# Optimization experiments

Measured on AMD Instinct MI355X. Metric: run time of the kernel, lower is better.

## Reference

```python
import jax, jax.numpy as jnp
import numpy as np

N_TOKENS = 16384
DIM = 7168
N_EXPERTS = 256
N_GROUPS = 8
TOPK_GROUPS = 4
TOPK = 8
ROUTE_SCALE = 2.5


def setup_inputs() -> dict:
    key = jax.random.key(0)
    k1, k2 = jax.random.split(key)
    x = jax.random.normal(k1, (N_TOKENS, DIM), dtype=jnp.float32)
    # kaiming_uniform_(a=sqrt(5)) -> Uniform(-1/sqrt(fan_in), 1/sqrt(fan_in))
    bound = 1.0 / np.sqrt(DIM)
    weight = jax.random.uniform(k2, (N_EXPERTS, DIM), dtype=jnp.float32,
                                minval=-bound, maxval=bound)
    expert_bias = jnp.zeros((N_EXPERTS,), dtype=jnp.float32)
    return {"x": x, "weight": weight, "expert_bias": expert_bias}


def reference(x, weight, expert_bias):
    n = x.shape[0]
    # linear scoring + sigmoid (score_func == 'sigmoid')
    scores = jax.nn.sigmoid(x @ weight.T)            # [n, E]
    biased = scores + expert_bias                    # [n, E]
    # group-limited routing
    bg = biased.reshape(n, N_GROUPS, -1)             # [n, G, E/G]
    top2, _ = jax.lax.top_k(bg, 2)
    group_scores = top2.sum(axis=-1)                 # [n, G]
    _, top_group_idx = jax.lax.top_k(group_scores, TOPK_GROUPS)  # [n, TOPK_GROUPS]
    keep = jax.nn.one_hot(top_group_idx, N_GROUPS, dtype=jnp.float32).sum(axis=1) > 0  # [n, G]
    masked = jnp.where(keep[:, :, None], bg, -jnp.inf).reshape(n, -1)  # [n, E]
    # final top-k over allowed experts
    _, indices = jax.lax.top_k(masked, TOPK)         # [n, TOPK]
    weights = jnp.take_along_axis(scores, indices, axis=1)
    weights = weights / (weights.sum(axis=-1, keepdims=True) + 1e-20)
    weights = weights * ROUTE_SCALE
    return weights.astype(x.dtype), indices
```

## Files before the change

kernel.cpp:

```cpp
#include <hip/hip_runtime.h>
#include <math.h>

#define MTOK 16384
#define NEXP 256
#define KDIM 7168

#define CAPR 1024
#define KSPLIT 8
#define KCH (KDIM / KSPLIT)
#define TAU 2e-5f

typedef _Float16 f16;
typedef __attribute__((ext_vector_type(8))) f16 f16x8;
typedef __attribute__((ext_vector_type(4))) f16 f16x4;
typedef __attribute__((ext_vector_type(4))) float f32x4;

#define BM 64
#define BN 128
#define BK 64
#define LDH 72

__launch_bounds__(256, 2)
__global__ void gemm_fp16x2_k(const float* __restrict__ X,
                              const float* __restrict__ W,
                              float* __restrict__ S) {
    __shared__ f16 Ahi[BM][LDH];
    __shared__ f16 Alo[BM][LDH];
    __shared__ f16 Bhi[BN][LDH];
    __shared__ f16 Blo[BN][LDH];

    const int tid  = threadIdx.x;
    const int lane = tid & 63;
    const int wid  = tid >> 6;
    const int wr   = wid >> 1;
    const int wc   = wid & 1;
    const int m0 = blockIdx.x * BM;
    const int n0 = blockIdx.y * BN;

    const int arow = tid >> 2;
    const int ac   = tid & 3;
    const int brow = tid >> 1;
    const int bc   = tid & 1;

    const float* xg = X + (size_t)(m0 + arow) * KDIM;
    const float* wg = W + (size_t)(n0 + brow) * KDIM;

    f32x4 accA[2][4];
    f32x4 accB[2][4];
#pragma unroll
    for (int i = 0; i < 2; ++i)
#pragma unroll
        for (int j = 0; j < 4; ++j) { accA[i][j] = (f32x4)0.f; accB[i][j] = (f32x4)0.f; }

    const int mr = wr * 32;
    const int nc = wc * 64;
    const int fr = lane & 15;
    const int fq = lane >> 4;

    for (int k0 = 0; k0 < KDIM; k0 += BK) {
        float4 av[4], bv[8];
#pragma unroll
        for (int i = 0; i < 4; ++i)
            av[i] = *(const float4*)(xg + k0 + (ac + i * 4) * 4);
#pragma unroll
        for (int i = 0; i < 8; ++i)
            bv[i] = *(const float4*)(wg + k0 + (bc + i * 2) * 4);

        __syncthreads();

#pragma unroll
        for (int i = 0; i < 4; ++i) {
            const int ke = (ac + i * 4) * 4;
            f16x4 h, l;
            h.x = (f16)av[i].x; l.x = (f16)((av[i].x - (float)h.x) * 2048.f);
            h.y = (f16)av[i].y; l.y = (f16)((av[i].y - (float)h.y) * 2048.f);
            h.z = (f16)av[i].z; l.z = (f16)((av[i].z - (float)h.z) * 2048.f);
            h.w = (f16)av[i].w; l.w = (f16)((av[i].w - (float)h.w) * 2048.f);
            *(f16x4*)&Ahi[arow][ke] = h;
            *(f16x4*)&Alo[arow][ke] = l;
        }
#pragma unroll
        for (int i = 0; i < 8; ++i) {
            const int ke = (bc + i * 2) * 4;
            f16x4 h, l;
            h.x = (f16)bv[i].x; l.x = (f16)((bv[i].x - (float)h.x) * 2048.f);
            h.y = (f16)bv[i].y; l.y = (f16)((bv[i].y - (float)h.y) * 2048.f);
            h.z = (f16)bv[i].z; l.z = (f16)((bv[i].z - (float)h.z) * 2048.f);
            h.w = (f16)bv[i].w; l.w = (f16)((bv[i].w - (float)h.w) * 2048.f);
            *(f16x4*)&Bhi[brow][ke] = h;
            *(f16x4*)&Blo[brow][ke] = l;
        }

        __syncthreads();

#pragma unroll
        for (int ks = 0; ks < 2; ++ks) {
            const int ke = ks * 32 + fq * 8;
            f16x8 ah[2], al[2], bh[4], bl[4];
#pragma unroll
            for (int mi = 0; mi < 2; ++mi) {
                ah[mi] = *(const f16x8*)&Ahi[mr + mi * 16 + fr][ke];
                al[mi] = *(const f16x8*)&Alo[mr + mi * 16 + fr][ke];
            }
#pragma unroll
            for (int ni = 0; ni < 4; ++ni) {
                bh[ni] = *(const f16x8*)&Bhi[nc + ni * 16 + fr][ke];
                bl[ni] = *(const f16x8*)&Blo[nc + ni * 16 + fr][ke];
            }
#pragma unroll
            for (int mi = 0; mi < 2; ++mi)
#pragma unroll
                for (int ni = 0; ni < 4; ++ni) {
                    accA[mi][ni] = __builtin_amdgcn_mfma_f32_16x16x32_f16(ah[mi], bh[ni], accA[mi][ni], 0, 0, 0);
                    accB[mi][ni] = __builtin_amdgcn_mfma_f32_16x16x32_f16(ah[mi], bl[ni], accB[mi][ni], 0, 0, 0);
                    accB[mi][ni] = __builtin_amdgcn_mfma_f32_16x16x32_f16(al[mi], bh[ni], accB[mi][ni], 0, 0, 0);
                }
        }
    }

#pragma unroll
    for (int mi = 0; mi < 2; ++mi)
#pragma unroll
        for (int ni = 0; ni < 4; ++ni) {
            const int e = n0 + nc + ni * 16 + fr;
#pragma unroll
            for (int r = 0; r < 4; ++r) {
                const int m = m0 + mr + mi * 16 + fq * 4 + r;
                float logit = accA[mi][ni][r] + accB[mi][ni][r] * (1.f / 2048.f);
                S[(size_t)m * NEXP + e] = 1.f / (1.f + expf(-logit));
            }
        }
}

__launch_bounds__(256)
__global__ void route_flag_k(const float* __restrict__ S,
                             const float* __restrict__ bias,
                             float* __restrict__ out,
                             int* __restrict__ list,
                             int* __restrict__ count) {
    __shared__ float sraw[4][256];
    const int wv   = threadIdx.x >> 6;
    const int lane = threadIdx.x & 63;
    const int token = blockIdx.x * 4 + wv;
    const float NINF = -__builtin_inff();
    const float PINF =  __builtin_inff();

    const float* row = S + (size_t)token * NEXP;
    float4 v = *(const float4*)(row + lane * 4);
    *(float4*)&sraw[wv][lane * 4] = v;

    const int e0 = lane * 4;
    float4 bi4 = *(const float4*)(bias + e0);
    float b0 = v.x + bi4.x;
    float b1 = v.y + bi4.y;
    float b2 = v.z + bi4.z;
    float b3 = v.w + bi4.w;

    bool flag = false;

    float m1 = b0, m2 = NINF;
    if (b1 > m1) { m2 = m1; m1 = b1; } else if (b1 > m2) m2 = b1;
    if (b2 > m1) { m2 = m1; m1 = b2; } else if (b2 > m2) m2 = b2;
    if (b3 > m1) { m2 = m1; m1 = b3; } else if (b3 > m2) m2 = b3;
#pragma unroll
    for (int w = 1; w <= 4; w <<= 1) {
        float o1 = __shfl_xor(m1, w);
        float o2 = __shfl_xor(m2, w);
        float nm1 = fmaxf(m1, o1);
        float nm2 = fmaxf(fminf(m1, o1), fmaxf(m2, o2));
        m1 = nm1; m2 = nm2;
    }
    const float gs = m1 + m2;
    const int g = lane >> 3;

    int rank = 0;
#pragma unroll
    for (int j = 0; j < 8; ++j) {
        float gj = __shfl(gs, j * 8);
        rank += (gj > gs) || (gj == gs && j < g);
    }
    const bool sel = rank < 4;

    {
        float a = sel ? gs : PINF;
        float b = sel ? NINF : gs;
#pragma unroll
        for (int w = 1; w < 64; w <<= 1) {
            a = fminf(a, __shfl_xor(a, w));
            b = fmaxf(b, __shfl_xor(b, w));
        }
        flag |= (a - b) < 2.f * TAU;
    }

    if (!sel) { b0 = NINF; b1 = NINF; b2 = NINF; b3 = NINF; }

    int myidx = 0;
    float prev = 0.f;
#pragma unroll
    for (int it = 0; it < 9; ++it) {
        float bv = b0; int bi = e0;
        if (b1 > bv) { bv = b1; bi = e0 + 1; }
        if (b2 > bv) { bv = b2; bi = e0 + 2; }
        if (b3 > bv) { bv = b3; bi = e0 + 3; }
#pragma unroll
        for (int w = 1; w < 64; w <<= 1) {
            float ov = __shfl_xor(bv, w);
            int   oi = __shfl_xor(bi, w);
            if (ov > bv || (ov == bv && oi < bi)) { bv = ov; bi = oi; }
        }
        if (it > 0) flag |= (prev - bv) < TAU;
        prev = bv;
        if (it < 8) {
            if (lane == it) myidx = bi;
            if ((bi >> 2) == lane) {
                switch (bi & 3) {
                    case 0: b0 = NINF; break;
                    case 1: b1 = NINF; break;
                    case 2: b2 = NINF; break;
                    case 3: b3 = NINF; break;
                }
            }
        }
    }

    const bool anyflag = __any((int)flag);

    __syncthreads();

    float wval = (lane < 8) ? sraw[wv][myidx] : 0.f;
    float s = wval;
    s += __shfl_xor(s, 1);
    s += __shfl_xor(s, 2);
    s += __shfl_xor(s, 4);
    if (lane < 8) {
        float wout = wval / (s + 1e-20f) * 2.5f;
        out[(size_t)token * 8 + lane] = wout;
        out[(size_t)MTOK * 8 + (size_t)token * 8 + lane] = (float)myidx;
    }

    if (anyflag && lane == 0) {
        int f = atomicAdd(count, 1);
        if (f < CAPR) list[f] = token;
    }
}

__launch_bounds__(256)
__global__ void rescore_k(const float* __restrict__ X,
                          const float* __restrict__ W,
                          const int* __restrict__ list,
                          const int* __restrict__ count,
                          double* __restrict__ Ldp) {
    const int cnt = min(*count, CAPR);
    const int m0 = blockIdx.x * 64;
    if (m0 >= cnt) return;
    const int n0 = blockIdx.y * 64;
    const int ks = blockIdx.z;
    const int kbase = ks * KCH;

    __shared__ float As[16][66];
    __shared__ float Bs[16][66];
    const int tid = threadIdx.x;
    const int row = tid >> 2;
    const int c   = tid & 3;
    const int tm  = tid >> 4;
    const int tn  = tid & 15;

    const int gi = list[min(m0 + row, cnt - 1)];
    const float* xg = X + (size_t)gi * KDIM + c * 4;
    const float* wg = W + (size_t)(n0 + row) * KDIM + c * 4;

    double acc[4][4];
#pragma unroll
    for (int i = 0; i < 4; ++i)
#pragma unroll
        for (int j = 0; j < 4; ++j) acc[i][j] = 0.0;

    for (int k0 = kbase; k0 < kbase + KCH; k0 += 16) {
        float4 a = *(const float4*)(xg + k0);
        float4 b = *(const float4*)(wg + k0);
        __syncthreads();
        As[c * 4 + 0][row] = a.x; As[c * 4 + 1][row] = a.y;
        As[c * 4 + 2][row] = a.z; As[c * 4 + 3][row] = a.w;
        Bs[c * 4 + 0][row] = b.x; Bs[c * 4 + 1][row] = b.y;
        Bs[c * 4 + 2][row] = b.z; Bs[c * 4 + 3][row] = b.w;
        __syncthreads();
#pragma unroll
        for (int k = 0; k < 16; ++k) {
            double ad[4], bd[4];
#pragma unroll
            for (int i = 0; i < 4; ++i) ad[i] = (double)As[k][tm * 4 + i];
#pragma unroll
            for (int j = 0; j < 4; ++j) bd[j] = (double)Bs[k][tn * 4 + j];
#pragma unroll
            for (int i = 0; i < 4; ++i)
#pragma unroll
                for (int j = 0; j < 4; ++j)
                    acc[i][j] = fma(ad[i], bd[j], acc[i][j]);
        }
    }

#pragma unroll
    for (int i = 0; i < 4; ++i) {
        const int r = m0 + tm * 4 + i;
        if (r < cnt) {
#pragma unroll
            for (int j = 0; j < 4; ++j)
                Ldp[((size_t)ks * CAPR + r) * NEXP + n0 + tn * 4 + j] = acc[i][j];
        }
    }
}

__launch_bounds__(64)
__global__ void route_exact_k(const double* __restrict__ Ldp,
                              const float* __restrict__ bias,
                              const int* __restrict__ list,
                              const int* __restrict__ count,
                              float* __restrict__ out) {
    const int cnt = min(*count, CAPR);
    const int f = blockIdx.x;
    if (f >= cnt) return;
    const int lane = threadIdx.x;
    const int token = list[f];
    const double NINF = -__builtin_inf();

    const int e0 = lane * 4;
    double l0 = 0.0, l1 = 0.0, l2 = 0.0, l3 = 0.0;
#pragma unroll
    for (int s = 0; s < KSPLIT; ++s) {
        double4 p = *(const double4*)(Ldp + ((size_t)s * CAPR + f) * NEXP + e0);
        l0 += p.x; l1 += p.y; l2 += p.z; l3 += p.w;
    }

    double s0 = 1.0 / (1.0 + exp(-l0));
    double s1 = 1.0 / (1.0 + exp(-l1));
    double s2 = 1.0 / (1.0 + exp(-l2));
    double s3 = 1.0 / (1.0 + exp(-l3));

    float4 bi4 = *(const float4*)(bias + e0);
    double b0 = s0 + (double)bi4.x;
    double b1 = s1 + (double)bi4.y;
    double b2 = s2 + (double)bi4.z;
    double b3 = s3 + (double)bi4.w;

    double m1 = b0, m2 = NINF;
    if (b1 > m1) { m2 = m1; m1 = b1; } else if (b1 > m2) m2 = b1;
    if (b2 > m1) { m2 = m1; m1 = b2; } else if (b2 > m2) m2 = b2;
    if (b3 > m1) { m2 = m1; m1 = b3; } else if (b3 > m2) m2 = b3;
#pragma unroll
    for (int w = 1; w <= 4; w <<= 1) {
        double o1 = __shfl_xor(m1, w);
        double o2 = __shfl_xor(m2, w);
        double nm1 = fmax(m1, o1);
        double nm2 = fmax(fmin(m1, o1), fmax(m2, o2));
        m1 = nm1; m2 = nm2;
    }
    const double gs = m1 + m2;
    const int g = lane >> 3;

    int rank = 0;
#pragma unroll
    for (int j = 0; j < 8; ++j) {
        double gj = __shfl(gs, j * 8);
        rank += (gj > gs) || (gj == gs && j < g);
    }
    if (rank >= 4) { b0 = NINF; b1 = NINF; b2 = NINF; b3 = NINF; }

    int myidx = 0;
#pragma unroll
    for (int it = 0; it < 8; ++it) {
        double bv = b0; int bi = e0;
        if (b1 > bv) { bv = b1; bi = e0 + 1; }
        if (b2 > bv) { bv = b2; bi = e0 + 2; }
        if (b3 > bv) { bv = b3; bi = e0 + 3; }
#pragma unroll
        for (int w = 1; w < 64; w <<= 1) {
            double ov = __shfl_xor(bv, w);
            int    oi = __shfl_xor(bi, w);
            if (ov > bv || (ov == bv && oi < bi)) { bv = ov; bi = oi; }
        }
        if (lane == it) myidx = bi;
        if ((bi >> 2) == lane) {
            switch (bi & 3) {
                case 0: b0 = NINF; break;
                case 1: b1 = NINF; break;
                case 2: b2 = NINF; break;
                case 3: b3 = NINF; break;
            }
        }
    }

    double g0 = __shfl(s0, myidx >> 2);
    double g1 = __shfl(s1, myidx >> 2);
    double g2 = __shfl(s2, myidx >> 2);
    double g3 = __shfl(s3, myidx >> 2);
    const int ss = myidx & 3;
    double wval = (lane < 8) ? (ss == 0 ? g0 : ss == 1 ? g1 : ss == 2 ? g2 : g3) : 0.0;
    double s = wval;
    s += __shfl_xor(s, 1);
    s += __shfl_xor(s, 2);
    s += __shfl_xor(s, 4);
    if (lane < 8) {
        float wout = (float)(wval / (s + 1e-20) * 2.5);
        out[(size_t)token * 8 + lane] = wout;
        out[(size_t)MTOK * 8 + (size_t)token * 8 + lane] = (float)myidx;
    }
}

__global__ void init_k(int* count) { *count = 0; }

extern "C" void kernel_launch(void* const* d_in, const int* in_sizes, int n_in,
                              void* d_out, int out_size, void* d_ws, size_t ws_size,
                              hipStream_t stream) {
    const float* X    = (const float*)d_in[0];
    const float* W    = (const float*)d_in[1];
    const float* bias = (const float*)d_in[2];
    float* out = (float*)d_out;

    float*  Lf   = (float*)d_ws;
    double* Ldp  = (double*)d_ws;
    int*    list = (int*)((char*)d_ws + 16777216);
    int*    cnt  = (int*)((char*)d_ws + 16777216 + CAPR * 4);

    init_k<<<1, 1, 0, stream>>>(cnt);

    dim3 g1(MTOK / BM, NEXP / BN);
    gemm_fp16x2_k<<<g1, 256, 0, stream>>>(X, W, Lf);

    route_flag_k<<<MTOK / 4, 256, 0, stream>>>(Lf, bias, out, list, cnt);

    dim3 g3(CAPR / 64, NEXP / 64, KSPLIT);
    rescore_k<<<g3, 256, 0, stream>>>(X, W, list, cnt, Ldp);

    route_exact_k<<<CAPR, 64, 0, stream>>>(Ldp, bias, list, cnt, out);
}
```

Baseline: 454.9 us.

## Pre-split weights into fp16 MFMA fragment layout and double-buffer A tiles

A new kernel converts the weight matrix once per call into hi/lo fp16 halves stored in MFMA-fragment order, so the GEMM reads B straight from global memory into registers without LDS staging or per-tile conversion. The GEMM now stages only the X tile in double-buffered LDS with one barrier per k-step, and uses an XCD-aware block index remap so blocks sharing W sit on the same XCD. The goal is to cut redundant W conversion, LDS traffic and synchronization. In exchange it adds an extra launch and a workspace buffer, and the GEMM now has a fixed grid of 512 blocks.

```diff
diff --git a/kernel.cpp b/kernel.cpp
--- a/kernel.cpp
+++ b/kernel.cpp
@@ -10,40 +10,68 @@
 #define KCH (KDIM / KSPLIT)
 #define TAU 2e-5f
 
+#define NKC 224
+#define WFRAG_ELEMS ((size_t)2 * 16 * NKC * 512)
+
 typedef _Float16 f16;
 typedef __attribute__((ext_vector_type(8))) f16 f16x8;
-typedef __attribute__((ext_vector_type(4))) f16 f16x4;
 typedef __attribute__((ext_vector_type(4))) float f32x4;
 
-#define BM 64
-#define BN 128
-#define BK 64
-#define LDH 72
+__global__ void wconv_k(const float* __restrict__ W, f16* __restrict__ Wfrag) {
+    const int e  = blockIdx.x;
+    const int kc = threadIdx.x;
+    if (kc >= NKC) return;
+    const int nt  = e >> 4;
+    const int col = e & 15;
+    const float* src = W + (size_t)e * KDIM + kc * 32;
+    float x[32];
+#pragma unroll
+    for (int i = 0; i < 8; ++i) {
+        float4 v = *(const float4*)(src + i * 4);
+        x[i * 4 + 0] = v.x; x[i * 4 + 1] = v.y; x[i * 4 + 2] = v.z; x[i * 4 + 3] = v.w;
+    }
+#pragma unroll
+    for (int k8 = 0; k8 < 4; ++k8) {
+        f16x8 h, l;
+#pragma unroll
+        for (int j = 0; j < 8; ++j) {
+            float xv = x[k8 * 8 + j];
+            f16 hh = (f16)xv;
+            h[j] = hh;
+            l[j] = (f16)((xv - (float)hh) * 2048.f);
+        }
+        const size_t lanepos = (size_t)(k8 * 16 + col) * 8;
+        *(f16x8*)(Wfrag + (((size_t)(0 * 16 + nt) * NKC + kc) << 9) + lanepos) = h;
+        *(f16x8*)(Wfrag + (((size_t)(1 * 16 + nt) * NKC + kc) << 9) + lanepos) = l;
+    }
+}
 
 __launch_bounds__(256, 2)
-__global__ void gemm_fp16x2_k(const float* __restrict__ X,
-                              const float* __restrict__ W,
-                              float* __restrict__ S) {
-    __shared__ f16 Ahi[BM][LDH];
-    __shared__ f16 Alo[BM][LDH];
-    __shared__ f16 Bhi[BN][LDH];
-    __shared__ f16 Blo[BN][LDH];
+__global__ void gemm_v7_k(const float* __restrict__ X,
+                          const f16* __restrict__ Wfrag,
+                          float* __restrict__ S) {
+    __shared__ f16 A_lds[2][2][4][64][8];
 
     const int tid  = threadIdx.x;
     const int lane = tid & 63;
-    const int wid  = tid >> 6;
-    const int wr   = wid >> 1;
-    const int wc   = wid & 1;
-    const int m0 = blockIdx.x * BM;
-    const int n0 = blockIdx.y * BN;
-
-    const int arow = tid >> 2;
-    const int ac   = tid & 3;
-    const int brow = tid >> 1;
-    const int bc   = tid & 1;
-
-    const float* xg = X + (size_t)(m0 + arow) * KDIM;
-    const float* wg = W + (size_t)(n0 + brow) * KDIM;
+    const int w    = tid >> 6;
+    const int wr   = w >> 1;
+    const int wc   = w & 1;
+
+    const int id   = blockIdx.x;
+    const int xcd  = id & 7;
+    const int slot = id >> 3;
+    const int nb   = xcd >> 2;
+    const int mb   = slot * 4 + (xcd & 3);
+    const int m0 = mb * 64;
+    const int n0 = nb * 128;
+
+    const int arow = tid & 63;
+    const int ak8  = tid >> 6;
+    const float* xg = X + (size_t)(m0 + arow) * KDIM + ak8 * 8;
+
+    const int fr = lane & 15;
+    const int fq = lane >> 4;
 
     f32x4 accA[2][4];
     f32x4 accB[2][4];
@@ -52,84 +80,87 @@
 #pragma unroll
         for (int j = 0; j < 4; ++j) { accA[i][j] = (f32x4)0.f; accB[i][j] = (f32x4)0.f; }
 
-    const int mr = wr * 32;
-    const int nc = wc * 64;
-    const int fr = lane & 15;
-    const int fq = lane >> 4;
-
-    for (int k0 = 0; k0 < KDIM; k0 += BK) {
-        float4 av[4], bv[8];
-#pragma unroll
-        for (int i = 0; i < 4; ++i)
-            av[i] = *(const float4*)(xg + k0 + (ac + i * 4) * 4);
-#pragma unroll
-        for (int i = 0; i < 8; ++i)
-            bv[i] = *(const float4*)(wg + k0 + (bc + i * 2) * 4);
-
+    float4 aA0, aA1, aB0, aB1;
+    f16x8 bh[4], bl[4];
+
+#define STORE_A(BUF_, R0_, R1_) do {                                        \
+        float xs_[8] = {(R0_).x, (R0_).y, (R0_).z, (R0_).w,                 \
+                        (R1_).x, (R1_).y, (R1_).z, (R1_).w};                \
+        f16x8 h_, l_;                                                       \
+        _Pragma("unroll")                                                   \
+        for (int e_ = 0; e_ < 8; ++e_) {                                    \
+            f16 hh_ = (f16)xs_[e_];                                         \
+            h_[e_] = hh_;                                                   \
+            l_[e_] = (f16)((xs_[e_] - (float)hh_) * 2048.f);                \
+        }                                                                   \
+        *(f16x8*)&A_lds[BUF_][0][ak8][arow][0] = h_;                        \
+        *(f16x8*)&A_lds[BUF_][1][ak8][arow][0] = l_;                        \
+    } while (0)
+
+#define B_LOADS(KC_) do {                                                   \
+        _Pragma("unroll")                                                   \
+        for (int ni_ = 0; ni_ < 4; ++ni_) {                                 \
+            const size_t nt_ = (size_t)(nb * 8 + wc * 4 + ni_);             \
+            bh[ni_] = *(const f16x8*)(Wfrag + (((nt_)      * NKC + (KC_)) << 9) + lane * 8); \
+            bl[ni_] = *(const f16x8*)(Wfrag + (((nt_ + 16) * NKC + (KC_)) << 9) + lane * 8); \
+        }                                                                   \
+    } while (0)
+
+#define COMPUTE(BUF_) do {                                                  \
+        f16x8 ah_[2], al_[2];                                               \
+        _Pragma("unroll")                                                   \
+        for (int mi_ = 0; mi_ < 2; ++mi_) {                                 \
+            const int r_ = wr * 32 + mi_ * 16 + fr;                         \
+            ah_[mi_] = *(const f16x8*)&A_lds[BUF_][0][fq][r_][0];           \
+            al_[mi_] = *(const f16x8*)&A_lds[BUF_][1][fq][r_][0];           \
+        }                                                                   \
+        _Pragma("unroll")                                                   \
+        for (int ni_ = 0; ni_ < 4; ++ni_) {                                 \
+            _Pragma("unroll")                                               \
+            for (int mi_ = 0; mi_ < 2; ++mi_) {                             \
+                accA[mi_][ni_] = __builtin_amdgcn_mfma_f32_16x16x32_f16(ah_[mi_], bh[ni_], accA[mi_][ni_], 0, 0, 0); \
+                accB[mi_][ni_] = __builtin_amdgcn_mfma_f32_16x16x32_f16(ah_[mi_], bl[ni_], accB[mi_][ni_], 0, 0, 0); \
+                accB[mi_][ni_] = __builtin_amdgcn_mfma_f32_16x16x32_f16(al_[mi_], bh[ni_], accB[mi_][ni_], 0, 0, 0); \
+            }                                                               \
+        }                                                                   \
+    } while (0)
+
+    aA0 = *(const float4*)(xg + 0);
+    aA1 = *(const float4*)(xg + 4);
+
+    for (int kc = 0; kc < NKC; kc += 2) {
+        STORE_A(0, aA0, aA1);
         __syncthreads();
-
-#pragma unroll
-        for (int i = 0; i < 4; ++i) {
-            const int ke = (ac + i * 4) * 4;
-            f16x4 h, l;
-            h.x = (f16)av[i].x; l.x = (f16)((av[i].x - (float)h.x) * 2048.f);
-            h.y = (f16)av[i].y; l.y = (f16)((av[i].y - (float)h.y) * 2048.f);
-            h.z = (f16)av[i].z; l.z = (f16)((av[i].z - (float)h.z) * 2048.f);
-            h.w = (f16)av[i].w; l.w = (f16)((av[i].w - (float)h.w) * 2048.f);
-            *(f16x4*)&Ahi[arow][ke] = h;
-            *(f16x4*)&Alo[arow][ke] = l;
-        }
-#pragma unroll
-        for (int i = 0; i < 8; ++i) {
-            const int ke = (bc + i * 2) * 4;
-            f16x4 h, l;
-            h.x = (f16)bv[i].x; l.x = (f16)((bv[i].x - (float)h.x) * 2048.f);
-            h.y = (f16)bv[i].y; l.y = (f16)((bv[i].y - (float)h.y) * 2048.f);
-            h.z = (f16)bv[i].z; l.z = (f16)((bv[i].z - (float)h.z) * 2048.f);
-            h.w = (f16)bv[i].w; l.w = (f16)((bv[i].w - (float)h.w) * 2048.f);
-            *(f16x4*)&Bhi[brow][ke] = h;
-            *(f16x4*)&Blo[brow][ke] = l;
-        }
-
+        aB0 = *(const float4*)(xg + (kc + 1) * 32 + 0);
+        aB1 = *(const float4*)(xg + (kc + 1) * 32 + 4);
+        B_LOADS(kc);
+        COMPUTE(0);
+
+        STORE_A(1, aB0, aB1);
         __syncthreads();
-
-#pragma unroll
-        for (int ks = 0; ks < 2; ++ks) {
-            const int ke = ks * 32 + fq * 8;
-            f16x8 ah[2], al[2], bh[4], bl[4];
-#pragma unroll
-            for (int mi = 0; mi < 2; ++mi) {
-                ah[mi] = *(const f16x8*)&Ahi[mr + mi * 16 + fr][ke];
-                al[mi] = *(const f16x8*)&Alo[mr + mi * 16 + fr][ke];
-            }
-#pragma unroll
-            for (int ni = 0; ni < 4; ++ni) {
-                bh[ni] = *(const f16x8*)&Bhi[nc + ni * 16 + fr][ke];
-                bl[ni] = *(const f16x8*)&Blo[nc + ni * 16 + fr][ke];
-            }
-#pragma unroll
-            for (int mi = 0; mi < 2; ++mi)
-#pragma unroll
-                for (int ni = 0; ni < 4; ++ni) {
-                    accA[mi][ni] = __builtin_amdgcn_mfma_f32_16x16x32_f16(ah[mi], bh[ni], accA[mi][ni], 0, 0, 0);
-                    accB[mi][ni] = __builtin_amdgcn_mfma_f32_16x16x32_f16(ah[mi], bl[ni], accB[mi][ni], 0, 0, 0);
-                    accB[mi][ni] = __builtin_amdgcn_mfma_f32_16x16x32_f16(al[mi], bh[ni], accB[mi][ni], 0, 0, 0);
-                }
-        }
+        if (kc + 2 < NKC) {
+            aA0 = *(const float4*)(xg + (kc + 2) * 32 + 0);
+            aA1 = *(const float4*)(xg + (kc + 2) * 32 + 4);
+        }
+        B_LOADS(kc + 1);
+        COMPUTE(1);
     }
 
 #pragma unroll
     for (int mi = 0; mi < 2; ++mi)
 #pragma unroll
         for (int ni = 0; ni < 4; ++ni) {
-            const int e = n0 + nc + ni * 16 + fr;
+            const int e = n0 + wc * 64 + ni * 16 + fr;
 #pragma unroll
             for (int r = 0; r < 4; ++r) {
-                const int m = m0 + mr + mi * 16 + fq * 4 + r;
+                const int m = m0 + wr * 32 + mi * 16 + fq * 4 + r;
                 float logit = accA[mi][ni][r] + accB[mi][ni][r] * (1.f / 2048.f);
                 S[(size_t)m * NEXP + e] = 1.f / (1.f + expf(-logit));
             }
         }
+#undef STORE_A
+#undef B_LOADS
+#undef COMPUTE
 }
 
 __launch_bounds__(256)
@@ -416,15 +447,16 @@
     const float* bias = (const float*)d_in[2];
     float* out = (float*)d_out;
 
-    float*  Lf   = (float*)d_ws;
-    double* Ldp  = (double*)d_ws;
-    int*    list = (int*)((char*)d_ws + 16777216);
-    int*    cnt  = (int*)((char*)d_ws + 16777216 + CAPR * 4);
+    float*  Lf    = (float*)d_ws;
+    double* Ldp   = (double*)d_ws;
+    int*    list  = (int*)((char*)d_ws + 16777216);
+    int*    cnt   = (int*)((char*)d_ws + 16777216 + CAPR * 4);
+    f16*    Wfrag = (f16*)((char*)d_ws + 16777216 + 65536);
 
     init_k<<<1, 1, 0, stream>>>(cnt);
-
-    dim3 g1(MTOK / BM, NEXP / BN);
-    gemm_fp16x2_k<<<g1, 256, 0, stream>>>(X, W, Lf);
+    wconv_k<<<NEXP, 256, 0, stream>>>(W, Wfrag);
+
+    gemm_v7_k<<<512, 256, 0, stream>>>(X, Wfrag, Lf);
 
     route_flag_k<<<MTOK / 4, 256, 0, stream>>>(Lf, bias, out, list, cnt);
 
```

Measured after the change: 653.2 us. 43.6% more time.
